# Performance work log

Measured on AMD Instinct MI355X. Metric: run time of the kernel, lower is better.

## Reference

```python
import jax, jax.numpy as jnp
import numpy as np

T, B, DIN, H, C = 32, 256, 4196, 1024, 151
DROP_P = 0.2


def setup_inputs() -> dict:
    key = jax.random.key(0)
    ks = jax.random.split(key, 9)
    x = jax.random.normal(ks[0], (T, B, DIN), dtype=jnp.float32)
    h0 = jnp.zeros((B, H), dtype=jnp.float32)
    c0 = jnp.zeros((B, H), dtype=jnp.float32)
    # recurrent dropout mask: binary mask scaled by 1/(1-p), sampled once, reused per step
    keep = (jax.random.uniform(ks[1], (B, H)) > DROP_P).astype(jnp.float32)
    dropout_mask = keep / (1.0 - DROP_P)
    s_in = 1.0 / np.sqrt(DIN)
    s_st = 1.0 / np.sqrt(H)
    W_in = jax.random.normal(ks[2], (6 * H, DIN), dtype=jnp.float32) * s_in
    b_in = jnp.zeros((6 * H,), dtype=jnp.float32)
    W_state = jax.random.normal(ks[3], (5 * H, H), dtype=jnp.float32) * s_st
    # bias init: zeros except forget-gate chunk = 1.0 (reset_parameters)
    b_state = jnp.zeros((5 * H,), dtype=jnp.float32).at[H:2 * H].set(1.0)
    W_out = jax.random.normal(ks[4], (C, H), dtype=jnp.float32) * s_st
    b_out = jnp.zeros((C,), dtype=jnp.float32)
    return {"x": x, "h0": h0, "c0": c0, "dropout_mask": dropout_mask,
            "W_in": W_in, "b_in": b_in, "W_state": W_state, "b_state": b_state,
            "W_out": W_out, "b_out": b_out}


def reference(x, h0, c0, dropout_mask, W_in, b_in, W_state, b_state, W_out, b_out):
    def step(carry, xt):
        h, c = carry
        pi = xt @ W_in.T + b_in            # [B, 6H]
        ps = h @ W_state.T + b_state       # [B, 5H]
        i_g = jax.nn.sigmoid(pi[:, 0 * H:1 * H] + ps[:, 0 * H:1 * H])
        f_g = jax.nn.sigmoid(pi[:, 1 * H:2 * H] + ps[:, 1 * H:2 * H])
        m_i = jnp.tanh(pi[:, 2 * H:3 * H] + ps[:, 2 * H:3 * H])
        o_g = jax.nn.sigmoid(pi[:, 3 * H:4 * H] + ps[:, 3 * H:4 * H])
        mem = i_g * m_i + f_g * c
        out = o_g * jnp.tanh(mem)
        hw = jax.nn.sigmoid(pi[:, 4 * H:5 * H] + ps[:, 4 * H:5 * H])
        out = hw * out + (1.0 - hw) * pi[:, 5 * H:6 * H]
        out = out * dropout_mask
        return (out, mem), out

    (_, _), hs = jax.lax.scan(step, (h0, c0), x)   # hs: [T, B, H]
    logits = jnp.einsum('tbh,ch->tbc', hs, W_out) + b_out
    return logits
```

## Files before the change

kernel.cpp:

```cpp
#include <hip/hip_runtime.h>
#include <hip/hip_bf16.h>
#include <cstdio>

typedef __bf16 bf16;
typedef __bf16 bf16x8 __attribute__((ext_vector_type(8)));
typedef __bf16 bf16x4 __attribute__((ext_vector_type(4)));
typedef float f32x4 __attribute__((ext_vector_type(4)));

__device__ __forceinline__ float sigmoidf_(float x) { return 1.f / (1.f + __expf(-x)); }
__device__ __forceinline__ float tanhf_(float x)    { return 1.f - 2.f / (__expf(2.f * x) + 1.f); }

__device__ __forceinline__ void gld_lds16(const bf16* g, bf16* l) {
    __builtin_amdgcn_global_load_lds(
        (const __attribute__((address_space(1))) void*)g,
        (__attribute__((address_space(3))) void*)l, 16, 0, 0);
}

__device__ __forceinline__ bf16x8 ldsfrag(const bf16* buf, int r, int kq) {
    int s = kq ^ (r & 7);
    return *(const bf16x8*)&buf[r * 64 + s * 8];
}

__device__ __forceinline__ void stage64(const bf16* src, int ld, int kk,
                                        bf16* dst, int r0, int tid) {
    int r  = r0 + (tid >> 3);
    int sl = tid & 7;
    int ks = (sl ^ (r & 7)) * 8;
    gld_lds16(src + (size_t)r * ld + kk + ks, dst + (r0 * 8 + tid) * 8);
}

__global__ __launch_bounds__(512)
void gemm256_k(const bf16* __restrict__ A, const bf16* __restrict__ B,
               bf16* __restrict__ C, const float* __restrict__ bias,
               int K, int lda, int ldb, int ldc, int nbx)
{
    __shared__ __align__(16) bf16 As[2][256 * 64];
    __shared__ __align__(16) bf16 Bs[2][256 * 64];

    const int tid  = threadIdx.x;
    const int wave = tid >> 6;
    const int lane = tid & 63;
    const int lrow = lane & 15;
    const int q    = lane >> 4;

    const int lb  = blockIdx.x;
    const int cpx = gridDim.x >> 3;
    const int swz = (lb & 7) * cpx + (lb >> 3);
    const int bx  = swz % nbx;
    const int by  = swz / nbx;

    const int rowbase = by * 256;
    const int colbase = bx * 256;
    const int wr = (wave >> 2) * 128;
    const int wc = (wave & 3) * 64;

    const bf16* Ab = A + (size_t)rowbase * lda;
    const bf16* Bb = B + (size_t)colbase * ldb;

    f32x4 acc[8][4] = {};
    const int NT = K >> 6;

#define G256_STAGE(ph, buf_, kk_)                                              \
    do {                                                                       \
        if ((ph) == 0) { stage64(Bb, ldb, (kk_), Bs[buf_],   0, tid);          \
                         stage64(Bb, ldb, (kk_), Bs[buf_],  64, tid); }        \
        if ((ph) == 1) { stage64(Bb, ldb, (kk_), Bs[buf_], 128, tid);          \
                         stage64(Bb, ldb, (kk_), Bs[buf_], 192, tid); }        \
        if ((ph) == 2) { stage64(Ab, lda, (kk_), As[buf_],   0, tid);          \
                         stage64(Ab, lda, (kk_), As[buf_], 128, tid); }        \
        if ((ph) == 3) { stage64(Ab, lda, (kk_), As[buf_],  64, tid);          \
                         stage64(Ab, lda, (kk_), As[buf_], 192, tid); }        \
    } while (0)

#define G256_PHASE(ph)                                                         \
    do {                                                                       \
        bf16x8 a00 = ldsfrag(Ac, wr + (2 * (ph) + 0) * 16 + lrow, q);          \
        bf16x8 a01 = ldsfrag(Ac, wr + (2 * (ph) + 0) * 16 + lrow, 4 | q);      \
        bf16x8 a10 = ldsfrag(Ac, wr + (2 * (ph) + 1) * 16 + lrow, q);          \
        bf16x8 a11 = ldsfrag(Ac, wr + (2 * (ph) + 1) * 16 + lrow, 4 | q);      \
        G256_STAGE(ph, nb, kkn);                                               \
        __builtin_amdgcn_s_barrier();                                          \
        __builtin_amdgcn_s_setprio(1);                                         \
        _Pragma("unroll")                                                      \
        for (int n_ = 0; n_ < 4; ++n_) {                                       \
            acc[2 * (ph) + 0][n_] = __builtin_amdgcn_mfma_f32_16x16x32_bf16(   \
                a00, bfr[n_][0], acc[2 * (ph) + 0][n_], 0, 0, 0);              \
            acc[2 * (ph) + 0][n_] = __builtin_amdgcn_mfma_f32_16x16x32_bf16(   \
                a01, bfr[n_][1], acc[2 * (ph) + 0][n_], 0, 0, 0);              \
            acc[2 * (ph) + 1][n_] = __builtin_amdgcn_mfma_f32_16x16x32_bf16(   \
                a10, bfr[n_][0], acc[2 * (ph) + 1][n_], 0, 0, 0);              \
            acc[2 * (ph) + 1][n_] = __builtin_amdgcn_mfma_f32_16x16x32_bf16(   \
                a11, bfr[n_][1], acc[2 * (ph) + 1][n_], 0, 0, 0);              \
        }                                                                      \
        __builtin_amdgcn_s_setprio(0);                                         \
    } while (0)

    G256_STAGE(0, 0, 0);
    G256_STAGE(1, 0, 0);
    G256_STAGE(2, 0, 0);
    G256_STAGE(3, 0, 0);
    asm volatile("s_waitcnt vmcnt(2)\n\ts_barrier" ::: "memory");

    for (int t = 0; t < NT; ++t) {
        const int cb  = t & 1;
        const int nb  = cb ^ 1;
        const int tn  = (t + 1 < NT) ? (t + 1) : t;
        const int kkn = tn << 6;
        const bf16* Ac = As[cb];
        const bf16* Bc = Bs[cb];

        bf16x8 bfr[4][2];
        #pragma unroll
        for (int n = 0; n < 4; ++n) {
            int rb = wc + n * 16 + lrow;
            bfr[n][0] = ldsfrag(Bc, rb, q);
            bfr[n][1] = ldsfrag(Bc, rb, 4 | q);
        }

        G256_PHASE(0);
        __builtin_amdgcn_s_barrier();
        G256_PHASE(1);
        asm volatile("s_waitcnt vmcnt(4)\n\ts_barrier" ::: "memory");
        G256_PHASE(2);
        __builtin_amdgcn_s_barrier();
        G256_PHASE(3);
        asm volatile("s_waitcnt vmcnt(2)\n\ts_barrier" ::: "memory");
    }
    asm volatile("s_waitcnt vmcnt(0)" ::: "memory");

#undef G256_PHASE
#undef G256_STAGE

    #pragma unroll
    for (int m = 0; m < 8; ++m) {
        #pragma unroll
        for (int n = 0; n < 4; ++n) {
            int gr0 = rowbase + wr + m * 16 + q * 4;
            int gc  = colbase + wc + n * 16 + lrow;
            float bv = bias[gc];
            #pragma unroll
            for (int rix = 0; rix < 4; ++rix)
                C[(size_t)(gr0 + rix) * ldc + gc] = (bf16)(acc[m][n][rix] + bv);
        }
    }
}

template<int BM, int BN, bool OUTBF16, bool NBOUND>
__global__ __launch_bounds__(256)
void gemm_lds_k(const bf16* __restrict__ A, const bf16* __restrict__ B,
                void* __restrict__ Cv, const float* __restrict__ bias,
                int K, int lda, int ldb, int ldc, int Nlim)
{
    constexpr int TM = BM / 32;
    constexpr int TN = BN / 32;

    __shared__ __align__(16) bf16 As[BM * 64];
    __shared__ __align__(16) bf16 Bs[BN * 64];

    const int tid  = threadIdx.x;
    const int wave = tid >> 6;
    const int lane = tid & 63;
    const int lrow = lane & 15;
    const int q    = lane >> 4;

    const int rowbase = blockIdx.y * BM;
    const int colbase = blockIdx.x * BN;
    const int wr = (wave >> 1) * (BM / 2);
    const int wc = (wave & 1) * (BN / 2);

    f32x4 acc[TM][TN] = {};

    for (int kk = 0; kk < K; kk += 64) {
        __syncthreads();
        #pragma unroll
        for (int i = 0; i < BM / 32; ++i) {
            int c  = tid + i * 256;
            int r  = c >> 3;
            int sl = c & 7;
            int ks = (sl ^ (r & 7)) * 8;
            gld_lds16(A + (size_t)(rowbase + r) * lda + kk + ks, &As[c * 8]);
        }
        #pragma unroll
        for (int i = 0; i < BN / 32; ++i) {
            int c  = tid + i * 256;
            int r  = c >> 3;
            int sl = c & 7;
            int ks = (sl ^ (r & 7)) * 8;
            gld_lds16(B + (size_t)(colbase + r) * ldb + kk + ks, &Bs[c * 8]);
        }
        __syncthreads();

        #pragma unroll
        for (int ks = 0; ks < 2; ++ks) {
            bf16x8 afr[TM], bfr[TN];
            #pragma unroll
            for (int m = 0; m < TM; ++m) {
                int r = wr + m * 16 + lrow;
                int s = ((ks << 2) | q) ^ (r & 7);
                afr[m] = *(const bf16x8*)&As[r * 64 + s * 8];
            }
            #pragma unroll
            for (int n = 0; n < TN; ++n) {
                int r = wc + n * 16 + lrow;
                int s = ((ks << 2) | q) ^ (r & 7);
                bfr[n] = *(const bf16x8*)&Bs[r * 64 + s * 8];
            }
            #pragma unroll
            for (int m = 0; m < TM; ++m)
                #pragma unroll
                for (int n = 0; n < TN; ++n)
                    acc[m][n] = __builtin_amdgcn_mfma_f32_16x16x32_bf16(
                                    afr[m], bfr[n], acc[m][n], 0, 0, 0);
        }
    }

    #pragma unroll
    for (int m = 0; m < TM; ++m) {
        #pragma unroll
        for (int n = 0; n < TN; ++n) {
            int gr0 = rowbase + wr + m * 16 + q * 4;
            int gc  = colbase + wc + n * 16 + lrow;
            bool cok = (!NBOUND) || (gc < Nlim);
            float bv = cok ? bias[gc] : 0.f;
            #pragma unroll
            for (int rix = 0; rix < 4; ++rix) {
                if (cok) {
                    float v = acc[m][n][rix] + bv;
                    size_t o = (size_t)(gr0 + rix) * ldc + gc;
                    if (OUTBF16) ((bf16*)Cv)[o] = (bf16)v;
                    else         ((float*)Cv)[o] = v;
                }
            }
        }
    }
}

template<int BM, int BN>
__global__ __launch_bounds__(256)
void gemm_cast_k(const float* __restrict__ Av, const float* __restrict__ Bv,
                 bf16* __restrict__ Cv, const float* __restrict__ bias,
                 int K, int Klim, int lda, int ldb, int ldc)
{
    constexpr int TM = BM / 32;
    constexpr int TN = BN / 32;
    constexpr int LDK = 40;

    __shared__ __align__(16) bf16 As[BM * LDK];
    __shared__ __align__(16) bf16 Bs[BN * LDK];

    const int tid  = threadIdx.x;
    const int wave = tid >> 6;
    const int lane = tid & 63;
    const int lrow = lane & 15;
    const int q    = lane >> 4;

    const int rowbase = blockIdx.y * BM;
    const int colbase = blockIdx.x * BN;
    const int wr = (wave >> 1) * (BM / 2);
    const int wc = (wave & 1) * (BN / 2);

    f32x4 acc[TM][TN] = {};

    for (int kk = 0; kk < K; kk += 32) {
        __syncthreads();
        #pragma unroll
        for (int i = 0; i < BM / 64; ++i) {
            int c = tid + i * 256;
            int r = c >> 2, kc = (c & 3) * 8, kg = kk + kc;
            const float* src = Av + (size_t)(rowbase + r) * lda + kg;
            bf16x8 v;
            if (kg + 8 <= Klim) {
                float4 f0 = *(const float4*)(src);
                float4 f1 = *(const float4*)(src + 4);
                v[0]=(bf16)f0.x; v[1]=(bf16)f0.y; v[2]=(bf16)f0.z; v[3]=(bf16)f0.w;
                v[4]=(bf16)f1.x; v[5]=(bf16)f1.y; v[6]=(bf16)f1.z; v[7]=(bf16)f1.w;
            } else {
                #pragma unroll
                for (int e = 0; e < 8; ++e) v[e] = (kg + e < Klim) ? (bf16)src[e] : (bf16)0.f;
            }
            *(bf16x8*)&As[r * LDK + kc] = v;
        }
        #pragma unroll
        for (int i = 0; i < BN / 64; ++i) {
            int c = tid + i * 256;
            int r = c >> 2, kc = (c & 3) * 8, kg = kk + kc;
            const float* src = Bv + (size_t)(colbase + r) * ldb + kg;
            bf16x8 v;
            if (kg + 8 <= Klim) {
                float4 f0 = *(const float4*)(src);
                float4 f1 = *(const float4*)(src + 4);
                v[0]=(bf16)f0.x; v[1]=(bf16)f0.y; v[2]=(bf16)f0.z; v[3]=(bf16)f0.w;
                v[4]=(bf16)f1.x; v[5]=(bf16)f1.y; v[6]=(bf16)f1.z; v[7]=(bf16)f1.w;
            } else {
                #pragma unroll
                for (int e = 0; e < 8; ++e) v[e] = (kg + e < Klim) ? (bf16)src[e] : (bf16)0.f;
            }
            *(bf16x8*)&Bs[r * LDK + kc] = v;
        }
        __syncthreads();

        bf16x8 afr[TM], bfr[TN];
        #pragma unroll
        for (int m = 0; m < TM; ++m)
            afr[m] = *(const bf16x8*)&As[(wr + m * 16 + lrow) * LDK + q * 8];
        #pragma unroll
        for (int n = 0; n < TN; ++n)
            bfr[n] = *(const bf16x8*)&Bs[(wc + n * 16 + lrow) * LDK + q * 8];
        #pragma unroll
        for (int m = 0; m < TM; ++m)
            #pragma unroll
            for (int n = 0; n < TN; ++n)
                acc[m][n] = __builtin_amdgcn_mfma_f32_16x16x32_bf16(
                                afr[m], bfr[n], acc[m][n], 0, 0, 0);
    }

    #pragma unroll
    for (int m = 0; m < TM; ++m) {
        #pragma unroll
        for (int n = 0; n < TN; ++n) {
            int gr0 = rowbase + wr + m * 16 + q * 4;
            int gc  = colbase + wc + n * 16 + lrow;
            float bv = bias[gc];
            #pragma unroll
            for (int rix = 0; rix < 4; ++rix)
                Cv[(size_t)(gr0 + rix) * ldc + gc] = (bf16)(acc[m][n][rix] + bv);
        }
    }
}

__global__ __launch_bounds__(512)
void step_k2(const bf16*  __restrict__ hprev,
             const bf16*  __restrict__ wsb,
             const bf16*  __restrict__ pi_t,
             const float* __restrict__ b_state,
             float*       __restrict__ cst,
             const float* __restrict__ dmask,
             bf16*        __restrict__ hnext)
{
    __shared__ __align__(16) unsigned char smem[36864];
    bf16* Asb = (bf16*)smem;
    bf16* Bsb = (bf16*)(smem + 16384);
    float* red = (float*)smem;

    const int tid   = threadIdx.x;
    const int wv    = tid >> 6;
    const int g2    = wv >> 2;
    const int wg    = wv & 3;
    const int lane  = tid & 63;
    const int lrow  = lane & 15;
    const int q     = lane >> 4;
    const int lt    = tid & 255;

    const int lb    = blockIdx.x;
    const int hb    = (lb >> 5) * 8 + (lb & 7);
    const int hbase = hb * 16;
    const int bbase = ((lb >> 3) & 3) * 64;
    const int kbase = g2 * 512;

    bf16* Ag = Asb + g2 * 4096;
    bf16* Bg = Bsb + g2 * 5120;

    const int b0   = bbase + wg * 16 + q * 4;
    const int hcol = hbase + lrow;
    bf16  pif[4][6];
    float crv[4], dmv[4], bsv[5];
    if (g2 == 0) {
        #pragma unroll
        for (int rix = 0; rix < 4; ++rix) {
            const bf16* pib = pi_t + (size_t)(b0 + rix) * 6144 + hcol;
            #pragma unroll
            for (int g = 0; g < 6; ++g) pif[rix][g] = pib[g * 1024];
            size_t j = (size_t)(b0 + rix) * 1024 + hcol;
            crv[rix] = cst[j];
            dmv[rix] = dmask[j];
        }
        #pragma unroll
        for (int g = 0; g < 5; ++g) bsv[g] = b_state[g * 1024 + hcol];
    }

    f32x4 acc[5] = {};
    for (int it = 0; it < 8; ++it) {
        const int kb = kbase + it * 64;
        __syncthreads();
        #pragma unroll
        for (int i = 0; i < 2; ++i) {
            int c  = lt + i * 256;
            int r  = c >> 3, sl = c & 7;
            int ks = (sl ^ (r & 7)) * 8;
            gld_lds16(hprev + (size_t)(bbase + r) * 1024 + kb + ks, Ag + c * 8);
        }
        #pragma unroll
        for (int i = 0; i < 3; ++i) {
            int c = lt + i * 256;
            if (c < 640) {
                int r  = c >> 3, sl = c & 7;
                int g  = r >> 4, hh = r & 15;
                int ks = (sl ^ (r & 7)) * 8;
                gld_lds16(wsb + (size_t)(g * 1024 + hbase + hh) * 1024 + kb + ks,
                          Bg + c * 8);
            }
        }
        __syncthreads();

        #pragma unroll
        for (int ks = 0; ks < 2; ++ks) {
            int ra = wg * 16 + lrow;
            int sa = ((ks << 2) | q) ^ (ra & 7);
            bf16x8 af = *(const bf16x8*)&Ag[ra * 64 + sa * 8];
            #pragma unroll
            for (int g = 0; g < 5; ++g) {
                int rb = g * 16 + lrow;
                int sb = ((ks << 2) | q) ^ (rb & 7);
                bf16x8 bv = *(const bf16x8*)&Bg[rb * 64 + sb * 8];
                acc[g] = __builtin_amdgcn_mfma_f32_16x16x32_bf16(af, bv, acc[g], 0, 0, 0);
            }
        }
    }

    __syncthreads();
    if (g2 == 1) {
        #pragma unroll
        for (int g = 0; g < 5; ++g)
            *(f32x4*)&red[(lt * 5 + g) * 4] = acc[g];
    }
    __syncthreads();
    if (g2 == 0) {
        #pragma unroll
        for (int g = 0; g < 5; ++g)
            acc[g] += *(const f32x4*)&red[(lt * 5 + g) * 4];

        #pragma unroll
        for (int rix = 0; rix < 4; ++rix) {
            int b = b0 + rix;
            float p0 = acc[0][rix] + bsv[0] + (float)pif[rix][0];
            float p1 = acc[1][rix] + bsv[1] + (float)pif[rix][1];
            float p2 = acc[2][rix] + bsv[2] + (float)pif[rix][2];
            float p3 = acc[3][rix] + bsv[3] + (float)pif[rix][3];
            float p4 = acc[4][rix] + bsv[4] + (float)pif[rix][4];
            float p5 = (float)pif[rix][5];

            float ig = sigmoidf_(p0);
            float fg = sigmoidf_(p1);
            float mi = tanhf_(p2);
            float og = sigmoidf_(p3);
            float hw = sigmoidf_(p4);

            size_t j = (size_t)b * 1024 + hcol;
            float mem = ig * mi + fg * crv[rix];
            cst[j] = mem;
            float out = og * tanhf_(mem);
            out = hw * out + (1.f - hw) * p5;
            out *= dmv[rix];
            hnext[j] = (bf16)out;
        }
    }
}

__global__ void cast_f2b4_k(const float* __restrict__ src, bf16* __restrict__ dst, int n4) {
    int i = blockIdx.x * 256 + threadIdx.x;
    if (i < n4) {
        float4 f = *(const float4*)(src + i * 4);
        bf16x4 v; v[0]=(bf16)f.x; v[1]=(bf16)f.y; v[2]=(bf16)f.z; v[3]=(bf16)f.w;
        *(bf16x4*)(dst + i * 4) = v;
    }
}

__global__ void cast_wout_k(const float* __restrict__ src, bf16* __restrict__ dst, int Crows) {
    int i = blockIdx.x * 256 + threadIdx.x;
    int r = i >> 10;
    dst[i] = (r < Crows) ? (bf16)src[i] : (bf16)0.f;
}

__global__ void cast_pad4_k(const float* __restrict__ src, bf16* __restrict__ dst,
                            int klim, int kp) {
    int r = blockIdx.x;
    const float* s = src + (size_t)r * klim;
    bf16* d = dst + (size_t)r * kp;
    int nk4 = kp >> 2, lim4 = klim >> 2;
    for (int c = threadIdx.x; c < nk4; c += 256) {
        bf16x4 v;
        if (c < lim4) {
            float4 f = *(const float4*)(s + c * 4);
            v[0]=(bf16)f.x; v[1]=(bf16)f.y; v[2]=(bf16)f.z; v[3]=(bf16)f.w;
        } else {
            v[0]=v[1]=v[2]=v[3]=(bf16)0.f;
        }
        *(bf16x4*)(d + c * 4) = v;
    }
}

__global__ void init_state_k(const float* __restrict__ c0, const float* __restrict__ h0,
                             float* __restrict__ cst, bf16* __restrict__ hs0) {
    int i = blockIdx.x * 256 + threadIdx.x;
    cst[i] = c0[i];
    hs0[i] = (bf16)h0[i];
}

extern "C" void kernel_launch(void* const* d_in, const int* in_sizes, int n_in,
                              void* d_out, int out_size, void* d_ws, size_t ws_size,
                              hipStream_t stream)
{
    const float* x       = (const float*)d_in[0];
    const float* h0      = (const float*)d_in[1];
    const float* c0      = (const float*)d_in[2];
    const float* dmask   = (const float*)d_in[3];
    const float* W_in    = (const float*)d_in[4];
    const float* b_in    = (const float*)d_in[5];
    const float* W_state = (const float*)d_in[6];
    const float* b_state = (const float*)d_in[7];
    const float* W_out   = (const float*)d_in[8];
    const float* b_out   = (const float*)d_in[9];

    constexpr int T = 32, B = 256, DIN = 4196, H = 1024, C = 151;
    constexpr int M  = T * B;
    constexpr int KP = 4224;
    constexpr int N6 = 6 * H;
    constexpr int N5 = 5 * H;

    size_t off = 0;
    auto carve = [&](size_t bytes) -> void* {
        void* p = (char*)d_ws + off;
        off += (bytes + 255) & ~(size_t)255;
        return p;
    };
    bf16*  pi  = (bf16*) carve((size_t)M * N6 * 2);
    bf16*  wsb = (bf16*) carve((size_t)N5 * H * 2);
    bf16*  wob = (bf16*) carve((size_t)192 * H * 2);
    bf16*  hs  = (bf16*) carve((size_t)(T + 1) * B * H * 2);
    float* cst = (float*)carve((size_t)B * H * 4);
    size_t base_need = off;

    bf16 *xb = nullptr, *wb = nullptr;
    bool precast = (ws_size >= base_need + (size_t)M * KP * 2 + (size_t)N6 * KP * 2 + 1024);
    if (precast) {
        xb = (bf16*)carve((size_t)M * KP * 2);
        wb = (bf16*)carve((size_t)N6 * KP * 2);
    }
    if (ws_size < base_need) {
        fprintf(stderr, "kernel_launch: ws too small (%zu < %zu)\n", ws_size, base_need);
        return;
    }

    hipLaunchKernelGGL(cast_f2b4_k, dim3((N5 * H / 4 + 255) / 256), dim3(256), 0, stream,
                       W_state, wsb, N5 * H / 4);
    hipLaunchKernelGGL(cast_wout_k, dim3(192 * H / 256), dim3(256), 0, stream, W_out, wob, C);
    hipLaunchKernelGGL(init_state_k, dim3(B * H / 256), dim3(256), 0, stream, c0, h0, cst, hs);

    if (precast) {
        hipLaunchKernelGGL(cast_pad4_k, dim3(M),  dim3(256), 0, stream, x,    xb, DIN, KP);
        hipLaunchKernelGGL(cast_pad4_k, dim3(N6), dim3(256), 0, stream, W_in, wb, DIN, KP);
        hipLaunchKernelGGL(gemm256_k,
                           dim3((M / 256) * (N6 / 256)), dim3(512), 0, stream,
                           xb, wb, pi, b_in, KP, KP, KP, N6, N6 / 256);
    } else {
        hipLaunchKernelGGL((gemm_cast_k<128, 128>),
                           dim3(N6 / 128, M / 128), dim3(256), 0, stream,
                           x, W_in, pi, b_in, KP, DIN, DIN, DIN, N6);
    }

    for (int t = 0; t < T; ++t) {
        hipLaunchKernelGGL(step_k2, dim3(256), dim3(512), 0, stream,
                           hs + (size_t)t * B * H, wsb,
                           pi + (size_t)t * B * N6, b_state,
                           cst, dmask,
                           hs + (size_t)(t + 1) * B * H);
    }

    hipLaunchKernelGGL((gemm_lds_k<128, 64, false, true>),
                       dim3(192 / 64, M / 128), dim3(256), 0, stream,
                       hs + (size_t)B * H, wob, (float*)d_out, b_out,
                       H, H, H, C, C);
}
```

Before: 1.103 ms.

## Double-buffer recurrent step loads and split work into smaller blocks

Result: no change. 1.081 ms (-1.9%).

```diff
diff --git a/kernel.cpp b/kernel.cpp
--- a/kernel.cpp
+++ b/kernel.cpp
@@ -328,8 +328,8 @@
     }
 }
 
-__global__ __launch_bounds__(512)
-void step_k2(const bf16*  __restrict__ hprev,
+__global__ __launch_bounds__(256)
+void step_k3(const bf16*  __restrict__ hprev,
              const bf16*  __restrict__ wsb,
              const bf16*  __restrict__ pi_t,
              const float* __restrict__ b_state,
@@ -337,28 +337,26 @@
              const float* __restrict__ dmask,
              bf16*        __restrict__ hnext)
 {
-    __shared__ __align__(16) unsigned char smem[36864];
-    bf16* Asb = (bf16*)smem;
-    bf16* Bsb = (bf16*)(smem + 16384);
+    __shared__ __align__(16) unsigned char smem[57344];
     float* red = (float*)smem;
 
     const int tid   = threadIdx.x;
     const int wv    = tid >> 6;
-    const int g2    = wv >> 2;
-    const int wg    = wv & 3;
+    const int g2    = wv >> 1;
+    const int wg    = wv & 1;
     const int lane  = tid & 63;
     const int lrow  = lane & 15;
     const int q     = lane >> 4;
-    const int lt    = tid & 255;
+    const int lt    = tid & 127;
 
     const int lb    = blockIdx.x;
-    const int hb    = (lb >> 5) * 8 + (lb & 7);
+    const int hb    = (lb >> 6) * 8 + (lb & 7);
     const int hbase = hb * 16;
-    const int bbase = ((lb >> 3) & 3) * 64;
+    const int bbase = ((lb >> 3) & 7) * 32;
     const int kbase = g2 * 512;
 
-    bf16* Ag = Asb + g2 * 4096;
-    bf16* Bg = Bsb + g2 * 5120;
+    bf16* Agrp = (bf16*)(smem + g2 * 28672);
+    bf16* Bgrp = (bf16*)(smem + g2 * 28672 + 8192);
 
     const int b0   = bbase + wg * 16 + q * 4;
     const int hcol = hbase + lrow;
@@ -378,44 +376,53 @@
         for (int g = 0; g < 5; ++g) bsv[g] = b_state[g * 1024 + hcol];
     }
 
+#define S3_STAGE(it_, bf_)                                                     \
+    do {                                                                       \
+        const int kb_ = kbase + (it_) * 64;                                    \
+        bf16* Ad_ = Agrp + (bf_) * 2048;                                       \
+        bf16* Bd_ = Bgrp + (bf_) * 5120;                                       \
+        _Pragma("unroll")                                                      \
+        for (int i_ = 0; i_ < 2; ++i_) {                                       \
+            int c_  = lt + i_ * 128;                                           \
+            int r_  = c_ >> 3, sl_ = c_ & 7;                                   \
+            int ks_ = (sl_ ^ (r_ & 7)) * 8;                                    \
+            gld_lds16(hprev + (size_t)(bbase + r_) * 1024 + kb_ + ks_,         \
+                      Ad_ + c_ * 8);                                           \
+        }                                                                      \
+        _Pragma("unroll")                                                      \
+        for (int i_ = 0; i_ < 5; ++i_) {                                       \
+            int c_  = lt + i_ * 128;                                           \
+            int r_  = c_ >> 3, sl_ = c_ & 7;                                   \
+            int g_  = r_ >> 4, hh_ = r_ & 15;                                  \
+            int ks_ = (sl_ ^ (r_ & 7)) * 8;                                    \
+            gld_lds16(wsb + (size_t)(g_ * 1024 + hbase + hh_) * 1024 + kb_ + ks_, \
+                      Bd_ + c_ * 8);                                           \
+        }                                                                      \
+    } while (0)
+
     f32x4 acc[5] = {};
+    S3_STAGE(0, 0);
+    asm volatile("s_waitcnt vmcnt(0)\n\ts_barrier" ::: "memory");
+
     for (int it = 0; it < 8; ++it) {
-        const int kb = kbase + it * 64;
-        __syncthreads();
-        #pragma unroll
-        for (int i = 0; i < 2; ++i) {
-            int c  = lt + i * 256;
-            int r  = c >> 3, sl = c & 7;
-            int ks = (sl ^ (r & 7)) * 8;
-            gld_lds16(hprev + (size_t)(bbase + r) * 1024 + kb + ks, Ag + c * 8);
-        }
-        #pragma unroll
-        for (int i = 0; i < 3; ++i) {
-            int c = lt + i * 256;
-            if (c < 640) {
-                int r  = c >> 3, sl = c & 7;
-                int g  = r >> 4, hh = r & 15;
-                int ks = (sl ^ (r & 7)) * 8;
-                gld_lds16(wsb + (size_t)(g * 1024 + hbase + hh) * 1024 + kb + ks,
-                          Bg + c * 8);
-            }
-        }
-        __syncthreads();
-
+        const int cur = it & 1;
+        if (it < 7) S3_STAGE(it + 1, cur ^ 1);
+
+        const bf16* Ac = Agrp + cur * 2048;
+        const bf16* Bc = Bgrp + cur * 5120;
+        const int ra = wg * 16 + lrow;
         #pragma unroll
         for (int ks = 0; ks < 2; ++ks) {
-            int ra = wg * 16 + lrow;
-            int sa = ((ks << 2) | q) ^ (ra & 7);
-            bf16x8 af = *(const bf16x8*)&Ag[ra * 64 + sa * 8];
+            bf16x8 af = ldsfrag(Ac, ra, (ks << 2) | q);
             #pragma unroll
             for (int g = 0; g < 5; ++g) {
-                int rb = g * 16 + lrow;
-                int sb = ((ks << 2) | q) ^ (rb & 7);
-                bf16x8 bv = *(const bf16x8*)&Bg[rb * 64 + sb * 8];
+                bf16x8 bv = ldsfrag(Bc, g * 16 + lrow, (ks << 2) | q);
                 acc[g] = __builtin_amdgcn_mfma_f32_16x16x32_bf16(af, bv, acc[g], 0, 0, 0);
             }
         }
-    }
+        asm volatile("s_waitcnt vmcnt(0)\n\ts_barrier" ::: "memory");
+    }
+#undef S3_STAGE
 
     __syncthreads();
     if (g2 == 1) {
@@ -559,7 +566,7 @@
     }
 
     for (int t = 0; t < T; ++t) {
-        hipLaunchKernelGGL(step_k2, dim3(256), dim3(512), 0, stream,
+        hipLaunchKernelGGL(step_k3, dim3(512), dim3(256), 0, stream,
                            hs + (size_t)t * B * H, wsb,
                            pi + (size_t)t * B * N6, b_state,
                            cst, dmask,
```
